# Kernel optimization log

Hardware: AMD Instinct MI355X
Metric: run time of the kernel (lower is better)

## Reference

```python
import jax, jax.numpy as jnp
import numpy as np
import math

L = 2          # gnn_num_layers
NDIM = 256     # gnn_hidden_size
H = 8          # num_heads
HH = H // 2    # heads per (full, local) split
DK = NDIM // H # 32, also == edim (relation_share_heads)
EDIM = DK
B, NPB = 32, 128
N = B * NPB            # 4096 nodes
EF = B * NPB * NPB     # 524288 complete-graph edges
EL = 131072            # local-graph edges
ELG = 262144           # line-graph edges
R = 128                # relation vocab


def _ln(x, g, b, eps=1e-5):
    m = x.mean(-1, keepdims=True)
    v = ((x - m) ** 2).mean(-1, keepdims=True)
    return (x - m) / jnp.sqrt(v + eps) * g + b


def _ffn(x, W1, b1, W2, b2, g, b):
    h = jax.nn.relu(x @ W1 + b1)
    return _ln(x + h @ W2 + b2, g, b)


def _edge_attn(q, k, v, e, src, dst, n_seg):
    """Relation-aware graph attention (DGL propagate_attention + edge_softmax).
    q,k,v: [n_seg,h,d]; e: [E,h,d] edge-relation bias or None; src,dst: [E].
    score_e = ((k[src]+e) . q[dst]) / sqrt(d); softmax over in-edges of dst;
    out[dst] = sum alpha_e * (v[src]+e)."""
    ks = k[src] + e if e is not None else k[src]          # [E,h,d]
    vs = v[src] + e if e is not None else v[src]          # [E,h,d]
    s = jnp.einsum('ehd,ehd->eh', ks, q[dst]) / math.sqrt(q.shape[-1])
    smax = jax.ops.segment_max(s, dst, num_segments=n_seg)
    ex = jnp.exp(s - jnp.maximum(smax, -1e30)[dst])
    den = jax.ops.segment_sum(ex, dst, num_segments=n_seg)[dst]
    alpha = ex / jnp.where(den > 0, den, 1.0)
    return jax.ops.segment_sum(alpha[..., None] * vs, dst, num_segments=n_seg)


def _model(x, rel_embed,
           n_Wq, n_bq, n_Wk, n_bk, n_Wv, n_bv, n_Wo, n_bo, n_ln_g, n_ln_b,
           n_f_W1, n_f_b1, n_f_W2, n_f_b2, n_f_ln_g, n_f_ln_b,
           e_Wsrc, e_Wdst, e_Wq, e_bq, e_Wk, e_Wv, e_Wo, e_bo, e_ln_g, e_ln_b,
           e_f_W1, e_f_b1, e_f_W2, e_f_b2, e_f_ln_g, e_f_ln_b,
           full_src, full_dst, g_src, g_dst, lg_src, lg_dst, edge_feat, full_edge_feat):
    lg_x = rel_embed[edge_feat]            # [EL, EDIM]  (shared embedding)
    lg_x_full = rel_embed[full_edge_feat]  # [EF, EDIM]  (fixed across layers)
    n, el, ef = x.shape[0], lg_x.shape[0], lg_x_full.shape[0]
    for i in range(L):
        # ---------- node update: first HH heads on full graph, last HH on local ----------
        q = (x @ n_Wq[i] + n_bq[i]).reshape(n, H, DK)
        k = (x @ n_Wk[i] + n_bk[i]).reshape(n, H, DK)
        v = (x @ n_Wv[i] + n_bv[i]).reshape(n, H, DK)
        # edim == d_k -> relation bias broadcast across heads (the expand branch)
        e_full = jnp.broadcast_to(lg_x_full[:, None, :], (ef, HH, DK))
        e_loc = jnp.broadcast_to(lg_x[:, None, :], (el, HH, DK))
        o1 = _edge_attn(q[:, :HH], k[:, :HH], v[:, :HH], e_full, full_src, full_dst, n)
        o2 = _edge_attn(q[:, HH:], k[:, HH:], v[:, HH:], e_loc, g_src, g_dst, n)
        o = jnp.concatenate([o1, o2], axis=1).reshape(n, NDIM)
        x_new = _ln(x + o @ n_Wo[i] + n_bo[i], n_ln_g[i], n_ln_b[i])
        x_new = _ffn(x_new, n_f_W1[i], n_f_b1[i], n_f_W2[i], n_f_b2[i], n_f_ln_g[i], n_f_ln_b[i])
        # ---------- edge update on line graph, conditioned on PRE-update src/dst node feats ----------
        mixed = lg_x + x[g_src] @ e_Wsrc[i] + x[g_dst] @ e_Wdst[i]  # [EL, EDIM]
        dke = EDIM // H
        eq = (mixed @ e_Wq[i] + e_bq[i]).reshape(el, H, dke)
        ek = (mixed @ e_Wk[i]).reshape(el, H, dke)
        ev = (mixed @ e_Wv[i]).reshape(el, H, dke)
        ow = _edge_attn(eq, ek, ev, None, lg_src, lg_dst, el).reshape(el, EDIM)
        lg_new = _ln(lg_x + ow @ e_Wo[i] + e_bo[i], e_ln_g[i], e_ln_b[i])
        lg_new = _ffn(lg_new, e_f_W1[i], e_f_b1[i], e_f_W2[i], e_f_b2[i], e_f_ln_g[i], e_f_ln_b[i])
        x, lg_x = x_new, lg_new
    return x, lg_x


def setup_inputs() -> dict:
    key = jax.random.key(0)
    ki = iter(jax.random.split(key, 48))
    def p(shape, scale=0.05):
        return jax.random.normal(next(ki), shape, dtype=jnp.float32) * scale
    rng = np.random.default_rng(0)
    blk = (np.arange(B, dtype=np.int32) * NPB)
    ii, jj = np.meshgrid(np.arange(NPB, dtype=np.int32), np.arange(NPB, dtype=np.int32), indexing='ij')
    full_src = (blk[:, None, None] + ii[None]).reshape(-1)   # block-diagonal complete graph
    full_dst = (blk[:, None, None] + jj[None]).reshape(-1)
    epb = EL // B
    g_src = (np.repeat(blk, epb) + rng.integers(0, NPB, EL)).astype(np.int32)
    g_dst = (np.repeat(blk, epb) + rng.integers(0, NPB, EL)).astype(np.int32)
    lpb = ELG // B
    eblk = np.arange(B, dtype=np.int32) * epb
    lg_src = (np.repeat(eblk, lpb) + rng.integers(0, epb, ELG)).astype(np.int32)
    lg_dst = (np.repeat(eblk, lpb) + rng.integers(0, epb, ELG)).astype(np.int32)
    return dict(
        x=jax.random.normal(next(ki), (N, NDIM), dtype=jnp.float32),
        rel_embed=p((R, EDIM), 1.0),
        full_src=jnp.asarray(full_src), full_dst=jnp.asarray(full_dst),
        g_src=jnp.asarray(g_src), g_dst=jnp.asarray(g_dst),
        lg_src=jnp.asarray(lg_src), lg_dst=jnp.asarray(lg_dst),
        edge_feat=jnp.asarray(rng.integers(0, R, EL).astype(np.int32)),
        full_edge_feat=jnp.asarray(rng.integers(0, R, EF).astype(np.int32)),
        n_Wq=p((L, NDIM, NDIM)), n_bq=p((L, NDIM)),
        n_Wk=p((L, NDIM, NDIM)), n_bk=p((L, NDIM)),
        n_Wv=p((L, NDIM, NDIM)), n_bv=p((L, NDIM)),
        n_Wo=p((L, NDIM, NDIM)), n_bo=p((L, NDIM)),
        n_ln_g=jnp.ones((L, NDIM), jnp.float32), n_ln_b=jnp.zeros((L, NDIM), jnp.float32),
        n_f_W1=p((L, NDIM, 4 * NDIM)), n_f_b1=p((L, 4 * NDIM)),
        n_f_W2=p((L, 4 * NDIM, NDIM)), n_f_b2=p((L, NDIM)),
        n_f_ln_g=jnp.ones((L, NDIM), jnp.float32), n_f_ln_b=jnp.zeros((L, NDIM), jnp.float32),
        e_Wsrc=p((L, NDIM, EDIM)), e_Wdst=p((L, NDIM, EDIM)),
        e_Wq=p((L, EDIM, EDIM)), e_bq=p((L, EDIM)),
        e_Wk=p((L, EDIM, EDIM)), e_Wv=p((L, EDIM, EDIM)),
        e_Wo=p((L, EDIM, EDIM)), e_bo=p((L, EDIM)),
        e_ln_g=jnp.ones((L, EDIM), jnp.float32), e_ln_b=jnp.zeros((L, EDIM), jnp.float32),
        e_f_W1=p((L, EDIM, 4 * EDIM)), e_f_b1=p((L, 4 * EDIM)),
        e_f_W2=p((L, 4 * EDIM, EDIM)), e_f_b2=p((L, EDIM)),
        e_f_ln_g=jnp.ones((L, EDIM), jnp.float32), e_f_ln_b=jnp.zeros((L, EDIM), jnp.float32),
    )


def reference(x, rel_embed, full_src, full_dst, g_src, g_dst, lg_src, lg_dst,
              edge_feat, full_edge_feat,
              n_Wq, n_bq, n_Wk, n_bk, n_Wv, n_bv, n_Wo, n_bo, n_ln_g, n_ln_b,
              n_f_W1, n_f_b1, n_f_W2, n_f_b2, n_f_ln_g, n_f_ln_b,
              e_Wsrc, e_Wdst, e_Wq, e_bq, e_Wk, e_Wv, e_Wo, e_bo, e_ln_g, e_ln_b,
              e_f_W1, e_f_b1, e_f_W2, e_f_b2, e_f_ln_g, e_f_ln_b):
    return _model(x, rel_embed,
                  n_Wq, n_bq, n_Wk, n_bk, n_Wv, n_bv, n_Wo, n_bo, n_ln_g, n_ln_b,
                  n_f_W1, n_f_b1, n_f_W2, n_f_b2, n_f_ln_g, n_f_ln_b,
                  e_Wsrc, e_Wdst, e_Wq, e_bq, e_Wk, e_Wv, e_Wo, e_bo, e_ln_g, e_ln_b,
                  e_f_W1, e_f_b1, e_f_W2, e_f_b2, e_f_ln_g, e_f_ln_b,
                  full_src, full_dst, g_src, g_dst, lg_src, lg_dst, edge_feat, full_edge_feat)
```

## Files before the change

kernel.cpp:

```cpp
#include <hip/hip_runtime.h>
#include <hip/hip_bf16.h>

typedef __hip_bfloat16 bf16;
typedef unsigned short ush;

static constexpr int kN   = 4096;
static constexpr int kND  = 256;
static constexpr int kEL  = 131072;
static constexpr int kED  = 32;
static constexpr int kELG = 262144;
static constexpr int kL   = 2;
static constexpr int kQW  = 832;
static constexpr int kKV  = 576;
static constexpr float kScaleN = 0.17677669529663687f;

using frag_ab = __attribute__((ext_vector_type(8))) short;
using frag_cd = __attribute__((ext_vector_type(4))) float;

__device__ __forceinline__ float ldf(const void* p, size_t i, int isbf){
    return isbf ? __bfloat162float(((const bf16*)p)[i]) : ((const float*)p)[i];
}
__device__ __forceinline__ ush f2b(float f){ bf16 h = __float2bfloat16(f); return *(ush*)&h; }
__device__ __forceinline__ float b2f(ush u){ return __uint_as_float(((unsigned)u)<<16); }
__device__ __forceinline__ ush ldb(const void* p, size_t i, int isbf){
// ... 140 lines not shown
__global__ __launch_bounds__(256) void scan_blk2_k(
    const int* __restrict__ cntL, const int* __restrict__ cntG,
    int* __restrict__ rowL, int* __restrict__ rowG, int* __restrict__ bsum)
{
    __shared__ int s[256];
    const int t = threadIdx.x;
    const bool isL = blockIdx.x < 4;
    const int* cnt = isL ? cntL : cntG;
    int* out = isL ? rowL : rowG;
    const int blk = isL ? blockIdx.x : blockIdx.x - 4;
    const int n = isL ? kN : kEL;
    const int b0 = blk*1024;
    int v[4], pre[4], tsum = 0;
    #pragma unroll
    for (int j=0;j<4;++j){
        int idx = b0 + t*4 + j;
        v[j] = (idx < n) ? cnt[idx] : 0;
        pre[j] = tsum; tsum += v[j];
    }
    s[t] = tsum; __syncthreads();
    for (int off=1; off<256; off<<=1){
        int x = (t>=off) ? s[t-off] : 0;
        __syncthreads();
        s[t] += x;
        __syncthreads();
    }
    int texc = s[t] - tsum;
    #pragma unroll
    for (int j=0;j<4;++j){
        int idx = b0 + t*4 + j;
        if (idx < n) out[idx] = texc + pre[j];
    }
    if (t == 255) bsum[(isL ? 0 : 8) + blk] = s[255];
}
__global__ __launch_bounds__(256) void scan_top2_k(int* __restrict__ bsum){
    __shared__ int sL[256], sG[256];
    const int t = threadIdx.x;
    int vL = (t < 4)   ? bsum[t]     : 0;
    int vG = (t < 128) ? bsum[8 + t] : 0;
    sL[t] = vL; sG[t] = vG; __syncthreads();
    for (int off=1; off<256; off<<=1){
        int xL = (t>=off) ? sL[t-off] : 0;
        int xG = (t>=off) ? sG[t-off] : 0;
        __syncthreads();
        sL[t] += xL; sG[t] += xG;
        __syncthreads();
    }
    if (t < 4)   bsum[t]     = sL[t] - vL;
    if (t < 128) bsum[8 + t] = sG[t] - vG;
}
__global__ void scan_add2_k(int* __restrict__ rowL, int* __restrict__ rowG,
                            const int* __restrict__ bsum,
                            int* __restrict__ curL, int* __restrict__ curG){
    int g = blockIdx.x*256 + threadIdx.x;
    if (g < kN){ int v = rowL[g] + bsum[g >> 10]; rowL[g] = v; curL[g] = v; }
    else if (g < kN + kEL){ int gg = g - kN;
        int v = rowG[gg] + bsum[8 + (gg >> 10)]; rowG[gg] = v; curG[gg] = v; }
    if (g == 0){ rowL[kN] = kEL; rowG[kEL] = kELG; }
}
__global__ void fill2_k(const int* __restrict__ gd, const int* __restrict__ lgd,
                        int* __restrict__ curL, int* __restrict__ curG,
                        int* __restrict__ eidL, int* __restrict__ eidG){
    int g = blockIdx.x*256 + threadIdx.x;
    if (g < kEL){ int pos = atomicAdd(&curL[gd[g]], 1); eidL[pos] = g; }
    else if (g < kEL + kELG){ int gg = g - kEL;
        int pos = atomicAdd(&curG[lgd[gg]], 1); eidG[pos] = gg; }
}

__global__ __launch_bounds__(256) void mgemm_k(
    const float* __restrict__ A, const ush* __restrict__ WT,
    const void* __restrict__ bias, size_t boff,
    float* __restrict__ C, const int* __restrict__ flag,
    int M, int N, int K, int flags, ush* __restrict__ aux)
{
    __shared__ __align__(16) ush As[64*72];
    __shared__ __align__(16) ush Ws[64*72];
    const int isbf = *flag;
    const int t = threadIdx.x;
    const int m0 = blockIdx.y*64, n0 = blockIdx.x*64;
    const int wave = t>>6, lane = t&63;
    const int quad = lane>>4, l15 = lane&15;
    const int r = t>>3, kq = (t&7)*8;
    const bool abf = flags & 32;

    frag_cd acc[4];
    #pragma unroll
    for (int tl=0; tl<4; ++tl)
        #pragma unroll
        for (int j=0;j<4;++j) acc[tl][j] = 0.f;

    const float* ap0 = A + (size_t)(m0+r)*K + kq;
    const float* ap1 = A + (size_t)(m0+r+32)*K + kq;
    const ush*   ab0 = (const ush*)A + (size_t)(m0+r)*K + kq;
    const ush*   ab1 = (const ush*)A + (size_t)(m0+r+32)*K + kq;
    const ush*   wp0 = WT + (size_t)(n0+r)*K + kq;
    const ush*   wp1 = WT + (size_t)(n0+r+32)*K + kq;

    float4 a00,a01,a10,a11; uint4 av0,av1, wv0,wv1;
    auto loadT = [&](int kk){
        if (abf) { av0 = *(const uint4*)(ab0+kk); av1 = *(const uint4*)(ab1+kk); }
        else { a00 = *(const float4*)(ap0+kk); a01 = *(const float4*)(ap0+kk+4);
               a10 = *(const float4*)(ap1+kk); a11 = *(const float4*)(ap1+kk+4); }
        wv0 = *(const uint4*)(wp0+kk); wv1 = *(const uint4*)(wp1+kk);
    };
    loadT(0);

    for (int kk = 0; kk < K; kk += 64) {
        if (abf) {
            *(uint4*)&As[r*72 + kq]        = av0;
            *(uint4*)&As[(r+32)*72 + kq]   = av1;
        } else {
            *(ushort4*)&As[r*72 + kq]       = make_ushort4(f2b(a00.x),f2b(a00.y),f2b(a00.z),f2b(a00.w));
            *(ushort4*)&As[r*72 + kq + 4]   = make_ushort4(f2b(a01.x),f2b(a01.y),f2b(a01.z),f2b(a01.w));
            *(ushort4*)&As[(r+32)*72 + kq]     = make_ushort4(f2b(a10.x),f2b(a10.y),f2b(a10.z),f2b(a10.w));
            *(ushort4*)&As[(r+32)*72 + kq + 4] = make_ushort4(f2b(a11.x),f2b(a11.y),f2b(a11.z),f2b(a11.w));
        }
        *(uint4*)&Ws[r*72 + kq]      = wv0;
        *(uint4*)&Ws[(r+32)*72 + kq] = wv1;
        __syncthreads();
        if (kk + 64 < K) loadT(kk + 64);
        frag_ab af0 = *(const frag_ab*)&As[(wave*16 + l15)*72 + quad*8];
        frag_ab af1 = *(const frag_ab*)&As[(wave*16 + l15)*72 + 32 + quad*8];
        #pragma unroll
        for (int tl = 0; tl < 4; ++tl) {
            frag_ab bf0 = *(const frag_ab*)&Ws[(tl*16 + l15)*72 + quad*8];
            acc[tl] = __builtin_amdgcn_mfma_f32_16x16x32_bf16(af0, bf0, acc[tl], 0, 0, 0);
            frag_ab bf1 = *(const frag_ab*)&Ws[(tl*16 + l15)*72 + 32 + quad*8];
            acc[tl] = __builtin_amdgcn_mfma_f32_16x16x32_bf16(af1, bf1, acc[tl], 0, 0, 0);
        }
        __syncthreads();
    }
    const bool do_relu = flags & 2;
    const bool has_b   = flags & 4;
    const bool obf     = flags & 8;
    #pragma unroll
    for (int tl = 0; tl < 4; ++tl) {
        int col = n0 + tl*16 + l15;
        float bv = 0.f;
        if (has_b) bv = (flags & 16) ? ((const float*)bias)[boff + col]
                                     : ldf(bias, boff + col, isbf);
        #pragma unroll
        for (int rg = 0; rg < 4; ++rg) {
            int row = m0 + wave*16 + quad*4 + rg;
            float v = acc[tl][rg] + bv;
            if (do_relu) v = fmaxf(v, 0.f);
            if (flags & 64) {
                if (col < 256) C[(size_t)row*256 + col] = v;
                else           aux[(size_t)row*kKV + (col - 256)] = f2b(v);
            } else if (obf) ((ush*)C)[(size_t)row*N + col] = f2b(v);
            else            C[(size_t)row*N + col] = v;
        }
    }
}

__global__ __launch_bounds__(256) void ln_k(
    const float* __restrict__ a, const float* __restrict__ b,
    const void* __restrict__ g, const void* __restrict__ be, size_t goff,
    float* __restrict__ out, ush* __restrict__ outb,
    const int* __restrict__ flag, int D)
{
    const int isbf = *flag;
    const int row = blockIdx.x*4 + (threadIdx.x >> 6);
    const int t = threadIdx.x & 63;
    float v[4];
    int cnt = 0;
    float s = 0.f;
    for (int i = t; i < D; i += 64) {
        float x = a[(size_t)row*D + i];
        if (b) x += b[(size_t)row*D + i];
        v[cnt++] = x; s += x;
    }
    #pragma unroll
    for (int off = 32; off > 0; off >>= 1) s += __shfl_down(s, off);
    s = __shfl(s, 0);
    const float mean = s / D;
    float qq = 0.f;
    for (int c2 = 0; c2 < cnt; ++c2) { float d = v[c2]-mean; qq += d*d; }
    #pragma unroll
    for (int off = 32; off > 0; off >>= 1) qq += __shfl_down(qq, off);
    qq = __shfl(qq, 0);
    const float inv = rsqrtf(fmaxf(qq, 0.f) / D + 1e-5f);
    cnt = 0;
    for (int i = t; i < D; i += 64) {
        float r = (v[cnt++] - mean)*inv*ldf(g, goff + i, isbf) + ldf(be, goff + i, isbf);
        out[(size_t)row*D + i] = r;
        outb[(size_t)row*D + i] = f2b(r);
    }
}

__global__ __launch_bounds__(256) void eqkv_mfma_k(
    const ush* __restrict__ lg, const ush* __restrict__ kv,
    const int* __restrict__ gsrc, const int* __restrict__ gdst,
    const ush* __restrict__ WQKV, size_t woff,
    const void* __restrict__ bq, size_t boff,
    ush* __restrict__ eq, ush* __restrict__ ek, ush* __restrict__ ev,
    const int* __restrict__ flag)
{
    __shared__ __align__(16) ush mixs[128*40];
    __shared__ __align__(16) ush wts[3][32*40];
    __shared__ float bqs[32];
    const int isbf = *flag;
    const int t = threadIdx.x;
    const int e0 = blockIdx.x * 128;
    #pragma unroll
    for (int i = t; i < 768; i += 256) {
        int m = i >> 8, r2 = i & 255;
        int n = r2 >> 3, k4 = (r2 & 7) * 4;
        *(ushort4*)&wts[m][n*40 + k4] =
            *(const ushort4*)&WQKV[(size_t)m*2048 + woff + (size_t)n*32 + k4];
    }
    if (t < 32) bqs[t] = ldf(bq, boff + t, isbf);
    {
        int r = t >> 1, c0 = (t & 1) * 16;
        int e = e0 + r;
        int s = gsrc[e], d2 = gdst[e];
        const ush* lp = lg + (size_t)e*32 + c0;
        const ush* sp = kv + (size_t)s*kKV + 512 + c0;
        const ush* dp = kv + (size_t)d2*kKV + 544 + c0;
        #pragma unroll
        for (int j = 0; j < 16; ++j)
            mixs[r*40 + c0 + j] = f2b(b2f(lp[j]) + b2f(sp[j]) + b2f(dp[j]));
    }
    __syncthreads();
    const int wave = t >> 6, l15 = t & 15, quad = (t >> 4) & 3;
    #pragma unroll
    for (int mi = 0; mi < 2; ++mi) {
        const int mt = wave*2 + mi;
        frag_ab af = *(const frag_ab*)&mixs[(mt*16 + l15)*40 + quad*8];
        #pragma unroll
        for (int w = 0; w < 3; ++w) {
            ush* outp = (w==0) ? eq : ((w==1) ? ek : ev);
            #pragma unroll
            for (int nt = 0; nt < 2; ++nt) {
                frag_ab bf = *(const frag_ab*)&wts[w][(nt*16 + l15)*40 + quad*8];
                frag_cd acc = {0.f, 0.f, 0.f, 0.f};
                acc = __builtin_amdgcn_mfma_f32_16x16x32_bf16(af, bf, acc, 0, 0, 0);
                const float bv = (w==0) ? bqs[nt*16 + l15] : 0.f;
                #pragma unroll
                for (int rg = 0; rg < 4; ++rg) {
                    int row = e0 + mt*16 + quad*4 + rg;
                    outp[(size_t)row*32 + nt*16 + l15] = f2b(acc[rg] + bv);
                }
            }
        }
    }
}

__global__ __launch_bounds__(256) void effn_mfma_k(
    const ush* __restrict__ A,
    const ush* __restrict__ W1T, size_t w1off, const void* __restrict__ b1, size_t b1off,
    const ush* __restrict__ W2T, size_t w2off, const void* __restrict__ b2, size_t b2off,
    const void* __restrict__ g, const void* __restrict__ be, size_t goff,
    ush* __restrict__ out, const int* __restrict__ flag)
{
    __shared__ __align__(16) ush w1t[128*40];
    __shared__ __align__(16) ush w2t[32*136];
    __shared__ __align__(16) ush hid[64*136];
    __shared__ float b1s[128], b2s[32];
    const int isbf = *flag;
    const int t = threadIdx.x;
    const int wave = t >> 6, l15 = t & 15, quad = (t >> 4) & 3;

    #pragma unroll
    for (int i = t; i < 1024; i += 256) {
        int n1 = i >> 3, k4 = (i & 7) * 4;
        *(ushort4*)&w1t[n1*40 + k4] = *(const ushort4*)&W1T[w1off + (size_t)n1*32 + k4];
        int n2 = i >> 5, kq2 = (i & 31) * 4;
        *(ushort4*)&w2t[n2*136 + kq2] = *(const ushort4*)&W2T[w2off + (size_t)n2*128 + kq2];
    }
    if (t < 128) b1s[t] = ldf(b1, b1off + t, isbf);
    if (t < 32)  b2s[t] = ldf(b2, b2off + t, isbf);
    __syncthreads();

    const float g0  = ldf(g,  goff + l15, isbf),      g1v = ldf(g,  goff + 16 + l15, isbf);
    const float be0 = ldf(be, goff + l15, isbf),      be1 = ldf(be, goff + 16 + l15, isbf);
    const float bb0 = b2s[l15], bb1 = b2s[16 + l15];

    for (int tt = 0; tt < 2; ++tt) {
        const int e0 = (blockIdx.x*2 + tt) * 64;
        {
            const int m = wave*16 + l15;
            frag_ab af = *(const frag_ab*)&A[(size_t)(e0+m)*32 + quad*8];
            #pragma unroll
            for (int nt = 0; nt < 8; ++nt) {
                frag_ab bf = *(const frag_ab*)&w1t[(nt*16 + l15)*40 + quad*8];
                frag_cd acc = {0.f, 0.f, 0.f, 0.f};
                acc = __builtin_amdgcn_mfma_f32_16x16x32_bf16(af, bf, acc, 0, 0, 0);
                float bv = b1s[nt*16 + l15];
                #pragma unroll
                for (int rg = 0; rg < 4; ++rg) {
                    int row = wave*16 + quad*4 + rg;
                    hid[row*136 + nt*16 + l15] = f2b(fmaxf(acc[rg] + bv, 0.f));
                }
            }
        }
        frag_cd acc2[2] = {{0.f,0.f,0.f,0.f},{0.f,0.f,0.f,0.f}};
        #pragma unroll
        for (int ks = 0; ks < 4; ++ks) {
            frag_ab af2 = *(const frag_ab*)&hid[(wave*16 + l15)*136 + ks*32 + quad*8];
            #pragma unroll
            for (int tl = 0; tl < 2; ++tl) {
                frag_ab bf2 = *(const frag_ab*)&w2t[(tl*16 + l15)*136 + ks*32 + quad*8];
                acc2[tl] = __builtin_amdgcn_mfma_f32_16x16x32_bf16(af2, bf2, acc2[tl], 0, 0, 0);
            }
        }
        #pragma unroll
        for (int rg = 0; rg < 4; ++rg) {
            const int row = e0 + wave*16 + quad*4 + rg;
            float v0 = acc2[0][rg] + bb0 + b2f(A[(size_t)row*32 + l15]);
            float v1 = acc2[1][rg] + bb1 + b2f(A[(size_t)row*32 + 16 + l15]);
            float s = v0 + v1;
            s += __shfl_xor(s,1); s += __shfl_xor(s,2); s += __shfl_xor(s,4); s += __shfl_xor(s,8);
            const float mean = s * (1.f/32.f);
            float q = (v0-mean)*(v0-mean) + (v1-mean)*(v1-mean);
            q += __shfl_xor(q,1); q += __shfl_xor(q,2); q += __shfl_xor(q,4); q += __shfl_xor(q,8);
            const float inv = rsqrtf(q * (1.f/32.f) + 1e-5f);
            out[(size_t)row*32 + l15]      = f2b((v0-mean)*inv*g0  + be0);
            out[(size_t)row*32 + 16 + l15] = f2b((v1-mean)*inv*g1v + be1);
        }
    }
}

__global__ __launch_bounds__(512) void full_attn_k(
    const float* __restrict__ q, const ush* __restrict__ kv,
    const void* __restrict__ rel, const int* __restrict__ feat, ush* __restrict__ o,
    const int* __restrict__ flag)
{
    __shared__ __align__(8) ush ks[128][36];
    __shared__ __align__(8) ush vs[128][36];
    __shared__ __align__(8) ush rs[128][36];
    __shared__ float pb[8][32][34];
    const int isbf = *flag;
    const int bid = blockIdx.x;
    const int b = bid >> 4, h = (bid >> 2) & 3, qtr = bid & 3;
    const int t = threadIdx.x;
    for (int i = t; i < 4096; i += 512) {
        int r = i >> 5, d = i & 31;
        rs[r][d] = ldb(rel, i, isbf);
        const ush* kvrow = kv + (size_t)(b*128 + r)*kKV + h*32 + d;
        ks[r][d] = kvrow[0];
        vs[r][d] = kvrow[256];
    }
    __syncthreads();
    const int wave = t >> 6, lane = t & 63;
    const int dstL = lane >> 1, part = lane & 1;
    const int dst = qtr*32 + dstL;
    const int dbase = part*16;
    float qr[16];
    { size_t base = ((size_t)(b*128 + dst))*256 + h*32 + dbase;
      #pragma unroll
      for (int d=0; d<16; ++d) qr[d] = q[base + d]; }
    const int* fp = feat + (size_t)b*16384 + dst;
    const int s0 = wave*16;
    float m = -1e30f, l = 0.f;
    float acc[16];
    #pragma unroll
    for (int d=0; d<16; ++d) acc[d] = 0.f;
    int f = fp[s0*128];
    for (int sI = 0; sI < 16; ++sI) {
        const int s = s0 + sI;
        int fn = (sI+1 < 16) ? fp[(s+1)*128] : 0;
        float er[16];
        float scp = 0.f;
        #pragma unroll
        for (int j2 = 0; j2 < 4; ++j2) {
            ushort4 eu = *(const ushort4*)&rs[f][dbase + j2*4];
            ushort4 ku = *(const ushort4*)&ks[s][dbase + j2*4];
            float e0 = b2f(eu.x), e1 = b2f(eu.y), e2 = b2f(eu.z), e3 = b2f(eu.w);
            er[j2*4+0]=e0; er[j2*4+1]=e1; er[j2*4+2]=e2; er[j2*4+3]=e3;
            scp += (b2f(ku.x)+e0)*qr[j2*4+0] + (b2f(ku.y)+e1)*qr[j2*4+1]
                 + (b2f(ku.z)+e2)*qr[j2*4+2] + (b2f(ku.w)+e3)*qr[j2*4+3];
        }
        const float sc = (scp + __shfl_xor(scp, 1)) * kScaleN;
        float mn = fmaxf(m, sc);
        float c0 = __expf(m - mn);
        float pp = __expf(sc - mn);
        l = l*c0 + pp;
        #pragma unroll
        for (int j2 = 0; j2 < 4; ++j2) {
            ushort4 vu = *(const ushort4*)&vs[s][dbase + j2*4];
            acc[j2*4+0] = acc[j2*4+0]*c0 + pp*(b2f(vu.x)+er[j2*4+0]);
            acc[j2*4+1] = acc[j2*4+1]*c0 + pp*(b2f(vu.y)+er[j2*4+1]);
            acc[j2*4+2] = acc[j2*4+2]*c0 + pp*(b2f(vu.z)+er[j2*4+2]);
            acc[j2*4+3] = acc[j2*4+3]*c0 + pp*(b2f(vu.w)+er[j2*4+3]);
        }
        m = mn; f = fn;
    }
    if (part == 0) { pb[wave][dstL][0] = m; pb[wave][dstL][1] = l; }
    #pragma unroll
    for (int d=0; d<16; ++d) pb[wave][dstL][2 + dbase + d] = acc[d];
    __syncthreads();
    {
        const int dstL2 = t & 31, grp = t >> 5;
        float mw[8], lw[8];
        #pragma unroll
        for (int w=0; w<8; ++w){ mw[w]=pb[w][dstL2][0]; lw[w]=pb[w][dstL2][1]; }
        float M = mw[0];
        #pragma unroll
        for (int w=1; w<8; ++w) M = fmaxf(M, mw[w]);
        float sw[8];
        float L = 0.f;
        #pragma unroll
        for (int w=0; w<8; ++w){ sw[w] = __expf(mw[w]-M); L += lw[w]*sw[w]; }
        const float inv = 1.f / fmaxf(L, 1e-30f);
        size_t base = ((size_t)(b*128 + qtr*32 + dstL2))*kND + h*32 + grp*2;
        #pragma unroll
        for (int d=0; d<2; ++d) {
            float a = 0.f;
            #pragma unroll
            for (int w=0; w<8; ++w) a += pb[w][dstL2][2+grp*2+d]*sw[w];
            o[base + d] = f2b(a*inv);
        }
    }
}

__global__ __launch_bounds__(256) void loc_gather_k(
    const float* __restrict__ q, const ush* __restrict__ kv,
    const ush* __restrict__ lg, const int* __restrict__ gsrc,
    const int* __restrict__ rowp, const int* __restrict__ eidl,
    ush* __restrict__ o)
{
    const int n = blockIdx.x;
    const int h = threadIdx.x >> 6;
    const int lane = threadIdx.x & 63;
    const int g = lane >> 4;
    const int d0 = (lane & 15) * 2;
    const size_t hoff = (size_t)(4 + h) * 32 + d0;
    const float2 q2 = *(const float2*)&q[(size_t)n*256 + hoff];
    const int beg = rowp[n], end = rowp[n+1];
    const int deg = end - beg;
    float m = -1e30f, l = 0.f, ax = 0.f, ay = 0.f;
    if (deg > 0) {
        const int nIter = (deg + 3) >> 2;
        int idx = beg + g;
        int ce = eidl[min(idx, end-1)];
        int cs = gsrc[ce];
        for (int it = 0; it < nIter; ++it) {
            const bool valid = idx < end;
            const int e = ce, s = cs;
            idx += 4;
            if (it + 1 < nIter) { ce = eidl[min(idx, end-1)]; cs = gsrc[ce]; }
            const ushort2 ku = *(const ushort2*)&kv[(size_t)s*kKV + 128 + h*32 + d0];
            const ushort2 lvu = *(const ushort2*)&lg[(size_t)e*32 + d0];
            const ushort2 vu = *(const ushort2*)&kv[(size_t)s*kKV + 384 + h*32 + d0];
            const float lvx = b2f(lvu.x), lvy = b2f(lvu.y);
            float part = (b2f(ku.x)+lvx)*q2.x + (b2f(ku.y)+lvy)*q2.y;
            part += __shfl_xor(part, 1);
            part += __shfl_xor(part, 2);
            part += __shfl_xor(part, 4);
            part += __shfl_xor(part, 8);
            const float sc = part * kScaleN;
            const float mn = valid ? fmaxf(m, sc) : m;
            const float c  = __expf(m - mn);
            const float pp = valid ? __expf(sc - mn) : 0.f;
            l  = l*c  + pp;
            ax = ax*c + pp*(b2f(vu.x)+lvx);
            ay = ay*c + pp*(b2f(vu.y)+lvy);
            m  = mn;
        }
        #pragma unroll
        for (int off = 16; off <= 32; off <<= 1) {
            const float mo = __shfl_xor(m, off);
            const float lo = __shfl_xor(l, off);
            const float xo = __shfl_xor(ax, off);
            const float yo = __shfl_xor(ay, off);
            const float M  = fmaxf(m, mo);
            const float c1 = __expf(m - M);
            const float c2 = __expf(mo - M);
            l  = l*c1  + lo*c2;
            ax = ax*c1 + xo*c2;
            ay = ay*c1 + yo*c2;
            m  = M;
        }
    }
    if (g == 0) {
        const float inv = 1.f / fmaxf(l, 1e-30f);
        *(ushort2*)&o[(size_t)n*kND + hoff] = make_ushort2(f2b(ax*inv), f2b(ay*inv));
    }
}

__global__ __launch_bounds__(256) void lgs_ewo_k(
    const ush* __restrict__ eq, const ush* __restrict__ ek, const ush* __restrict__ ev,
    const int* __restrict__ lsrc, const int* __restrict__ rowp, const int* __restrict__ eidl,
    const ush* __restrict__ res,
    const ush* __restrict__ WO, size_t wooff, const void* __restrict__ bo, size_t booff,
    const void* __restrict__ g1, const void* __restrict__ be1, size_t g1off,
    ush* __restrict__ out, const int* __restrict__ flag)
{
    __shared__ __align__(16) ush ows[32*40];
    __shared__ __align__(16) ush wos[32*40];
    __shared__ float cs[32][36];
    __shared__ float bos[32], gs[32], bs[32];
    const int isbf = *flag;
    const int t = threadIdx.x;
    const int base = blockIdx.x * 32;
    {
        int n = t >> 3, k4 = (t & 7) * 4;
        *(ushort4*)&wos[n*40 + k4] = *(const ushort4*)&WO[wooff + (size_t)n*32 + k4];
    }
    if (t < 32) {
        bos[t] = ldf(bo, booff + t, isbf);
        gs[t]  = ldf(g1, g1off + t, isbf);
        bs[t]  = ldf(be1, g1off + t, isbf);
    }
    {
        const int d2 = base + (t >> 3), h = t & 7;
        const ushort4 qu = *(const ushort4*)&eq[(size_t)d2*32 + h*4];
        const float q0 = b2f(qu.x), q1 = b2f(qu.y), q2 = b2f(qu.z), q3 = b2f(qu.w);
        const int beg = rowp[d2], end = rowp[d2+1];
        float m = -1e30f, l = 0.f;
        float4 acc = make_float4(0.f,0.f,0.f,0.f);
        int i = beg;
        int s = 0;
        if (i < end) { s = lsrc[eidl[i]]; }
        while (i < end) {
            const int sc_s = s;
            ++i;
            if (i < end) { s = lsrc[eidl[i]]; }
            const ushort4 ku = *(const ushort4*)&ek[(size_t)sc_s*32 + h*4];
            const ushort4 vu = *(const ushort4*)&ev[(size_t)sc_s*32 + h*4];
            float sc = (b2f(ku.x)*q0 + b2f(ku.y)*q1 + b2f(ku.z)*q2 + b2f(ku.w)*q3) * 0.5f;
            float mn = fmaxf(m, sc);
            float c = __expf(m - mn);
            float pp = __expf(sc - mn);
            l = l*c + pp;
            acc.x = acc.x*c + pp*b2f(vu.x);
            acc.y = acc.y*c + pp*b2f(vu.y);
            acc.z = acc.z*c + pp*b2f(vu.z);
            acc.w = acc.w*c + pp*b2f(vu.w);
            m = mn;
        }
        const float inv = 1.f / fmaxf(l, 1e-30f);
        const int r = t >> 3, c0 = h*4;
        ows[r*40 + c0 + 0] = f2b(acc.x*inv);
        ows[r*40 + c0 + 1] = f2b(acc.y*inv);
        ows[r*40 + c0 + 2] = f2b(acc.z*inv);
        ows[r*40 + c0 + 3] = f2b(acc.w*inv);
    }
    __syncthreads();
    {
        const int wave = t >> 6, l15 = t & 15, quad = (t >> 4) & 3;
        const int mt = wave & 1, nt = wave >> 1;
        frag_ab af = *(const frag_ab*)&ows[(mt*16 + l15)*40 + quad*8];
        frag_ab bf = *(const frag_ab*)&wos[(nt*16 + l15)*40 + quad*8];
        frag_cd acc = {0.f, 0.f, 0.f, 0.f};
        acc = __builtin_amdgcn_mfma_f32_16x16x32_bf16(af, bf, acc, 0, 0, 0);
        #pragma unroll
        for (int rg = 0; rg < 4; ++rg) {
            const int row = mt*16 + quad*4 + rg;
            const int col = nt*16 + l15;
            cs[row][col] = acc[rg] + bos[col] + b2f(res[(size_t)(base+row)*32 + col]);
        }
    }
    __syncthreads();
    {
        const int row = t >> 3, c0 = (t & 7) * 4;
        const float v0 = cs[row][c0], v1 = cs[row][c0+1];
        const float v2 = cs[row][c0+2], v3 = cs[row][c0+3];
        float s = v0+v1+v2+v3;
        s += __shfl_xor(s,1); s += __shfl_xor(s,2); s += __shfl_xor(s,4);
        const float mean = s * (1.f/32.f);
        float qq = (v0-mean)*(v0-mean)+(v1-mean)*(v1-mean)
                 + (v2-mean)*(v2-mean)+(v3-mean)*(v3-mean);
        qq += __shfl_xor(qq,1); qq += __shfl_xor(qq,2); qq += __shfl_xor(qq,4);
        const float inv = rsqrtf(qq * (1.f/32.f) + 1e-5f);
        out[(size_t)(base+row)*32 + c0 + 0] = f2b((v0-mean)*inv*gs[c0+0] + bs[c0+0]);
        out[(size_t)(base+row)*32 + c0 + 1] = f2b((v1-mean)*inv*gs[c0+1] + bs[c0+1]);
        out[(size_t)(base+row)*32 + c0 + 2] = f2b((v2-mean)*inv*gs[c0+2] + bs[c0+2]);
        out[(size_t)(base+row)*32 + c0 + 3] = f2b((v3-mean)*inv*gs[c0+3] + bs[c0+3]);
    }
}

__global__ void out_k(const float* __restrict__ xf, const ush* __restrict__ lgf,
                      void* __restrict__ out, const int* __restrict__ flag){
    const int isbf = *flag;
    int g = blockIdx.x*256 + threadIdx.x;
    if (g < kN*kND) {
        float v = xf[g];
        if (isbf) ((ush*)out)[g] = f2b(v);
        else      ((float*)out)[g] = v;
    } else {
        ush u = lgf[g - kN*kND];
        if (isbf) ((ush*)out)[g] = u;
        else      ((float*)out)[g] = b2f(u);
    }
}

static inline void mgemm(const float* A, const ush* WT, const void* bias, size_t boff,
                         float* C, const int* flag, int M, int N, int K, int flags,
                         hipStream_t s, ush* aux){
    dim3 grid((N+63)/64, M/64);
    mgemm_k<<<grid, 256, 0, s>>>(A, WT, bias, boff, C, flag, M, N, K, flags, aux);
}

extern "C" void kernel_launch(void* const* d_in, const int* in_sizes, int n_in,
                              void* d_out, int out_size, void* d_ws, size_t ws_size,
                              hipStream_t stream) {
    const void* x_in      = d_in[0];
    const void* rel       = d_in[1];
    const int* g_src      = (const int*)d_in[4];
    const int* g_dst      = (const int*)d_in[5];
    const int* lg_src     = (const int*)d_in[6];
    const int* lg_dst     = (const int*)d_in[7];
    const int* edge_feat  = (const int*)d_in[8];
    const int* full_feat  = (const int*)d_in[9];
    const void* n_Wq   = d_in[10];
    const void* n_bq   = d_in[11];
    const void* n_Wk   = d_in[12];
    const void* n_bk   = d_in[13];
    const void* n_Wv   = d_in[14];
    const void* n_bv   = d_in[15];
    const void* n_Wo   = d_in[16];
    const void* n_bo   = d_in[17];
    const void* n_lng  = d_in[18];
    const void* n_lnb  = d_in[19];
    const void* n_fW1  = d_in[20];
    const void* n_fb1  = d_in[21];
    const void* n_fW2  = d_in[22];
    const void* n_fb2  = d_in[23];
    const void* n_flng = d_in[24];
    const void* n_flnb = d_in[25];
    const void* e_Wsrc = d_in[26];
    const void* e_Wdst = d_in[27];
    const void* e_Wq   = d_in[28];
    const void* e_bq   = d_in[29];
    const void* e_Wk   = d_in[30];
    const void* e_Wv   = d_in[31];
    const void* e_Wo   = d_in[32];
    const void* e_bo   = d_in[33];
    const void* e_lng  = d_in[34];
    const void* e_lnb  = d_in[35];
    const void* e_fW1  = d_in[36];
    const void* e_fb1  = d_in[37];
    const void* e_fW2  = d_in[38];
    const void* e_fb2  = d_in[39];
    const void* e_flng = d_in[40];
    const void* e_flnb = d_in[41];

    float* p = (float*)d_ws;
    size_t off = 0;
    auto AL = [&](size_t n){ float* r = p + off; off += n; return r; };
    int* flagp = (int*)AL(64);
    float* xA   = AL((size_t)kN*kND);
    float* xB   = AL((size_t)kN*kND);
    float* xM   = AL((size_t)kN*kND);
    ush*   xAb  = (ush*)AL((size_t)kN*kND/2);
    ush*   xBb  = (ush*)AL((size_t)kN*kND/2);
    ush*   xMb  = (ush*)AL((size_t)kN*kND/2);
    float* qkvb = AL((size_t)kN*kND);
    ush*   kvaux= (ush*)AL((size_t)kN*kKV/2);
    ush*   ob   = (ush*)AL((size_t)kN*kND/2);
    float* tN   = AL((size_t)kN*kND);
    ush*   nh   = (ush*)AL((size_t)kN*512);
    ush*   lgA  = (ush*)AL((size_t)kEL*kED/2);
    ush*   lgB  = (ush*)AL((size_t)kEL*kED/2);
    ush*   lgM  = (ush*)AL((size_t)kEL*kED/2);
    ush*   eqb  = (ush*)AL((size_t)kEL*16);
    ush*   ekb  = (ush*)AL((size_t)kEL*16);
    ush*   evb  = (ush*)AL((size_t)kEL*16);
    int* cntL  = (int*)AL(kN);
    int* rowL  = (int*)AL(kN + 64);
    int* curL  = (int*)AL(kN);
    int* eidL  = (int*)AL(kEL);
    int* cntG  = (int*)AL(kEL);
    int* rowG  = (int*)AL(kEL + 64);
    int* curG  = (int*)AL(kEL);
    int* eidG  = (int*)AL(kELG);
    int* bsum  = (int*)AL(256);
    ush* wtQKVSD = (ush*)AL(212992);
    float* bQKV  = AL(2*kQW);
    ush* wtO  = (ush*)AL(65536);
    ush* wtF1 = (ush*)AL(262144);
    ush* wtF2 = (ush*)AL(262144);
    ush* wtEQKV = (ush*)AL(3072);
    ush* wtEO   = (ush*)AL(1024);
    ush* wtEF1  = (ush*)AL(4096);
    ush* wtEF2  = (ush*)AL(4096);
    if (ws_size < off * sizeof(float)) return;

    detect_k<<<1, 64, 0, stream>>>((const ush*)x_in, flagp);
    {
        long total = (long)kN*kND + (long)kEL*kED + 2*kQW + kN + kEL;
        int blocks = (int)((total + 255) / 256);
        setup_misc_k<<<blocks, 256, 0, stream>>>(x_in, rel, edge_feat, n_bq, n_bk, n_bv,
                                                 xA, xAb, lgA, bQKV, cntL, cntG, flagp);
    }
    trans_all_k<<<6368, 256, 0, stream>>>(n_Wq, n_Wk, n_Wv, n_Wo, n_fW1, n_fW2,
                                          e_Wsrc, e_Wdst, e_Wq, e_Wk, e_Wv, e_Wo,
                                          e_fW1, e_fW2, flagp,
                                          wtQKVSD, wtO, wtF1, wtF2,
                                          wtEQKV, wtEO, wtEF1, wtEF2);

    count2_k<<<(kEL+kELG)/256, 256, 0, stream>>>(g_dst, lg_dst, cntL, cntG);
    scan_blk2_k<<<132, 256, 0, stream>>>(cntL, cntG, rowL, rowG, bsum);
    scan_top2_k<<<1, 256, 0, stream>>>(bsum);
    scan_add2_k<<<(kN+kEL)/256, 256, 0, stream>>>(rowL, rowG, bsum, curL, curG);
    fill2_k<<<(kEL+kELG)/256, 256, 0, stream>>>(g_dst, lg_dst, curL, curG, eidL, eidG);

    float* xc = xA;  float* xn = xB;
    ush* xcb = xAb;  ush* xnb = xBb;
    ush* lgc = lgA;  ush* lgn = lgB;

    for (int i = 0; i < kL; ++i) {
        const size_t o256 = (size_t)i*kND;
        const size_t o1024= (size_t)i*1024;
        const size_t o32  = (size_t)i*kED;
        const size_t o128 = (size_t)i*128;

        mgemm((const float*)xcb, wtQKVSD + (size_t)i*212992, bQKV, (size_t)i*kQW, qkvb,
              flagp, kN, kQW, kND, 4|16|32|64, stream, kvaux);
        full_attn_k<<<512, 512, 0, stream>>>(qkvb, kvaux, rel, full_feat, ob, flagp);
        loc_gather_k<<<kN, 256, 0, stream>>>(qkvb, kvaux, lgc, g_src, rowL, eidL, ob);
        mgemm((const float*)ob, wtO + (size_t)i*65536, n_bo, o256, tN, flagp,
              kN, kND, kND, 4|32, stream, nullptr);
        ln_k<<<kN/4, 256, 0, stream>>>(xc, tN, n_lng, n_lnb, o256, xM, xMb, flagp, kND);
        mgemm((const float*)xMb, wtF1 + (size_t)i*262144, n_fb1, o1024, (float*)nh, flagp,
              kN, 1024, kND, 4|2|8|32, stream, nullptr);
        mgemm((const float*)nh, wtF2 + (size_t)i*262144, n_fb2, o256, tN, flagp,
              kN, kND, 1024, 4|32, stream, nullptr);
        ln_k<<<kN/4, 256, 0, stream>>>(xM, tN, n_flng, n_flnb, o256, xn, xnb, flagp, kND);

        eqkv_mfma_k<<<kEL/128, 256, 0, stream>>>(lgc, kvaux, g_src, g_dst,
                                                 wtEQKV, (size_t)i*1024, e_bq, o32,
                                                 eqb, ekb, evb, flagp);
        lgs_ewo_k<<<kEL/32, 256, 0, stream>>>(eqb, ekb, evb, lg_src, rowG, eidG,
                                              lgc, wtEO, (size_t)i*1024, e_bo, o32,
                                              e_lng, e_lnb, o32, lgM, flagp);
        effn_mfma_k<<<kEL/128, 256, 0, stream>>>(lgM, wtEF1, (size_t)i*4096, e_fb1, o128,
                                                 wtEF2, (size_t)i*4096, e_fb2, o32,
                                                 e_flng, e_flnb, o32, lgn, flagp);

        { float* t = xc; xc = xn; xn = t; }
        { ush* t = xcb; xcb = xnb; xnb = t; }
        { ush* t = lgc; lgc = lgn; lgn = t; }
    }

    out_k<<<(kN*kND + kEL*kED)/256, 256, 0, stream>>>(xc, lgc, d_out, flagp);
}
```

Measured before the change: 523.8 us.

## Split-K node GEMMs with partial sums reduced in layernorm; merge attention kernels

The output-projection and FFN2 node GEMMs (N=256, grid of 4x64=256 blocks) now use a split-K of 2 via blockIdx.z. Each half writes its partial sum to its own buffer, and the following layernorm adds both partials, so twice as many blocks run on the GPU without atomics. The full-graph and local-graph attention kernels are also merged into one launch, saving one launch and letting the two block types overlap. In exchange the workspace grows by one extra fp32 buffer, the layernorm reads more data, and the merged kernel gives the local blocks full-attention shared-memory and 512-thread occupancy limits.

```diff
diff --git a/kernel.cpp b/kernel.cpp
--- a/kernel.cpp
+++ b/kernel.cpp
@@ -246,6 +246,9 @@
     const int quad = lane>>4, l15 = lane&15;
     const int r = t>>3, kq = (t&7)*8;
     const bool abf = flags & 32;
+    const bool spk = flags & 128;
+    const int Kc   = spk ? (K / gridDim.z) : K;
+    const int koff = spk ? (blockIdx.z * Kc) : 0;
 
     frag_cd acc[4];
     #pragma unroll
@@ -253,12 +256,12 @@
         #pragma unroll
         for (int j=0;j<4;++j) acc[tl][j] = 0.f;
 
-    const float* ap0 = A + (size_t)(m0+r)*K + kq;
-    const float* ap1 = A + (size_t)(m0+r+32)*K + kq;
-    const ush*   ab0 = (const ush*)A + (size_t)(m0+r)*K + kq;
-    const ush*   ab1 = (const ush*)A + (size_t)(m0+r+32)*K + kq;
-    const ush*   wp0 = WT + (size_t)(n0+r)*K + kq;
-    const ush*   wp1 = WT + (size_t)(n0+r+32)*K + kq;
+    const float* ap0 = A + (size_t)(m0+r)*K + koff + kq;
+    const float* ap1 = A + (size_t)(m0+r+32)*K + koff + kq;
+    const ush*   ab0 = (const ush*)A + (size_t)(m0+r)*K + koff + kq;
+    const ush*   ab1 = (const ush*)A + (size_t)(m0+r+32)*K + koff + kq;
+    const ush*   wp0 = WT + (size_t)(n0+r)*K + koff + kq;
+    const ush*   wp1 = WT + (size_t)(n0+r+32)*K + koff + kq;
 
     float4 a00,a01,a10,a11; uint4 av0,av1, wv0,wv1;
     auto loadT = [&](int kk){
@@ -269,7 +272,7 @@
     };
     loadT(0);
 
-    for (int kk = 0; kk < K; kk += 64) {
+    for (int kk = 0; kk < Kc; kk += 64) {
         if (abf) {
             *(uint4*)&As[r*72 + kq]        = av0;
             *(uint4*)&As[(r+32)*72 + kq]   = av1;
@@ -282,7 +285,7 @@
         *(uint4*)&Ws[r*72 + kq]      = wv0;
         *(uint4*)&Ws[(r+32)*72 + kq] = wv1;
         __syncthreads();
-        if (kk + 64 < K) loadT(kk + 64);
+        if (kk + 64 < Kc) loadT(kk + 64);
         frag_ab af0 = *(const frag_ab*)&As[(wave*16 + l15)*72 + quad*8];
         frag_ab af1 = *(const frag_ab*)&As[(wave*16 + l15)*72 + 32 + quad*8];
         #pragma unroll
@@ -295,8 +298,9 @@
         __syncthreads();
     }
     const bool do_relu = flags & 2;
-    const bool has_b   = flags & 4;
+    const bool has_b   = (flags & 4) && (!spk || blockIdx.z == 0);
     const bool obf     = flags & 8;
+    float* Cz = spk ? (C + (size_t)blockIdx.z * M * N) : C;
     #pragma unroll
     for (int tl = 0; tl < 4; ++tl) {
         int col = n0 + tl*16 + l15;
@@ -312,13 +316,13 @@
                 if (col < 256) C[(size_t)row*256 + col] = v;
                 else           aux[(size_t)row*kKV + (col - 256)] = f2b(v);
             } else if (obf) ((ush*)C)[(size_t)row*N + col] = f2b(v);
-            else            C[(size_t)row*N + col] = v;
+            else            Cz[(size_t)row*N + col] = v;
         }
     }
 }
 
 __global__ __launch_bounds__(256) void ln_k(
-    const float* __restrict__ a, const float* __restrict__ b,
+    const float* __restrict__ a, const float* __restrict__ b, const float* __restrict__ b2,
     const void* __restrict__ g, const void* __restrict__ be, size_t goff,
     float* __restrict__ out, ush* __restrict__ outb,
     const int* __restrict__ flag, int D)
@@ -331,7 +335,8 @@
     float s = 0.f;
     for (int i = t; i < D; i += 64) {
         float x = a[(size_t)row*D + i];
-        if (b) x += b[(size_t)row*D + i];
+        if (b)  x += b[(size_t)row*D + i];
+        if (b2) x += b2[(size_t)row*D + i];
         v[cnt++] = x; s += x;
     }
     #pragma unroll
@@ -485,10 +490,12 @@
     }
 }
 
-__global__ __launch_bounds__(512) void full_attn_k(
+__global__ __launch_bounds__(512) void attn_all_k(
     const float* __restrict__ q, const ush* __restrict__ kv,
-    const void* __restrict__ rel, const int* __restrict__ feat, ush* __restrict__ o,
-    const int* __restrict__ flag)
+    const void* __restrict__ rel, const int* __restrict__ feat,
+    const ush* __restrict__ lg, const int* __restrict__ gsrc,
+    const int* __restrict__ rowp, const int* __restrict__ eidl,
+    ush* __restrict__ o, const int* __restrict__ flag)
 {
     __shared__ __align__(8) ush ks[128][36];
     __shared__ __align__(8) ush vs[128][36];
@@ -496,150 +503,145 @@
     __shared__ float pb[8][32][34];
     const int isbf = *flag;
     const int bid = blockIdx.x;
-    const int b = bid >> 4, h = (bid >> 2) & 3, qtr = bid & 3;
     const int t = threadIdx.x;
-    for (int i = t; i < 4096; i += 512) {
-        int r = i >> 5, d = i & 31;
-        rs[r][d] = ldb(rel, i, isbf);
-        const ush* kvrow = kv + (size_t)(b*128 + r)*kKV + h*32 + d;
-        ks[r][d] = kvrow[0];
-        vs[r][d] = kvrow[256];
-    }
-    __syncthreads();
-    const int wave = t >> 6, lane = t & 63;
-    const int dstL = lane >> 1, part = lane & 1;
-    const int dst = qtr*32 + dstL;
-    const int dbase = part*16;
-    float qr[16];
-    { size_t base = ((size_t)(b*128 + dst))*256 + h*32 + dbase;
-      #pragma unroll
-      for (int d=0; d<16; ++d) qr[d] = q[base + d]; }
-    const int* fp = feat + (size_t)b*16384 + dst;
-    const int s0 = wave*16;
-    float m = -1e30f, l = 0.f;
-    float acc[16];
-    #pragma unroll
-    for (int d=0; d<16; ++d) acc[d] = 0.f;
-    int f = fp[s0*128];
-    for (int sI = 0; sI < 16; ++sI) {
-        const int s = s0 + sI;
-        int fn = (sI+1 < 16) ? fp[(s+1)*128] : 0;
-        float er[16];
-        float scp = 0.f;
+    if (bid < 512) {
+        const int b = bid >> 4, h = (bid >> 2) & 3, qtr = bid & 3;
+        for (int i = t; i < 4096; i += 512) {
+            int r = i >> 5, d = i & 31;
+            rs[r][d] = ldb(rel, i, isbf);
+            const ush* kvrow = kv + (size_t)(b*128 + r)*kKV + h*32 + d;
+            ks[r][d] = kvrow[0];
+            vs[r][d] = kvrow[256];
+        }
+        __syncthreads();
+        const int wave = t >> 6, lane = t & 63;
+        const int dstL = lane >> 1, part = lane & 1;
+        const int dst = qtr*32 + dstL;
+        const int dbase = part*16;
+        float qr[16];
+        { size_t base = ((size_t)(b*128 + dst))*256 + h*32 + dbase;
+          #pragma unroll
+          for (int d=0; d<16; ++d) qr[d] = q[base + d]; }
+        const int* fp = feat + (size_t)b*16384 + dst;
+        const int s0 = wave*16;
+        float m = -1e30f, l = 0.f;
+        float acc[16];
         #pragma unroll
-        for (int j2 = 0; j2 < 4; ++j2) {
-            ushort4 eu = *(const ushort4*)&rs[f][dbase + j2*4];
-            ushort4 ku = *(const ushort4*)&ks[s][dbase + j2*4];
-            float e0 = b2f(eu.x), e1 = b2f(eu.y), e2 = b2f(eu.z), e3 = b2f(eu.w);
-            er[j2*4+0]=e0; er[j2*4+1]=e1; er[j2*4+2]=e2; er[j2*4+3]=e3;
-            scp += (b2f(ku.x)+e0)*qr[j2*4+0] + (b2f(ku.y)+e1)*qr[j2*4+1]
-                 + (b2f(ku.z)+e2)*qr[j2*4+2] + (b2f(ku.w)+e3)*qr[j2*4+3];
-        }
-        const float sc = (scp + __shfl_xor(scp, 1)) * kScaleN;
-        float mn = fmaxf(m, sc);
-        float c0 = __expf(m - mn);
-        float pp = __expf(sc - mn);
-        l = l*c0 + pp;
+        for (int d=0; d<16; ++d) acc[d] = 0.f;
+        int f = fp[s0*128];
+        for (int sI = 0; sI < 16; ++sI) {
+            const int s = s0 + sI;
+            int fn = (sI+1 < 16) ? fp[(s+1)*128] : 0;
+            float er[16];
+            float scp = 0.f;
+            #pragma unroll
+            for (int j2 = 0; j2 < 4; ++j2) {
+                ushort4 eu = *(const ushort4*)&rs[f][dbase + j2*4];
+                ushort4 ku = *(const ushort4*)&ks[s][dbase + j2*4];
+                float e0 = b2f(eu.x), e1 = b2f(eu.y), e2 = b2f(eu.z), e3 = b2f(eu.w);
+                er[j2*4+0]=e0; er[j2*4+1]=e1; er[j2*4+2]=e2; er[j2*4+3]=e3;
+                scp += (b2f(ku.x)+e0)*qr[j2*4+0] + (b2f(ku.y)+e1)*qr[j2*4+1]
+                     + (b2f(ku.z)+e2)*qr[j2*4+2] + (b2f(ku.w)+e3)*qr[j2*4+3];
+            }
+            const float sc = (scp + __shfl_xor(scp, 1)) * kScaleN;
+            float mn = fmaxf(m, sc);
+            float c0 = __expf(m - mn);
+            float pp = __expf(sc - mn);
+            l = l*c0 + pp;
+            #pragma unroll
+            for (int j2 = 0; j2 < 4; ++j2) {
+                ushort4 vu = *(const ushort4*)&vs[s][dbase + j2*4];
+                acc[j2*4+0] = acc[j2*4+0]*c0 + pp*(b2f(vu.x)+er[j2*4+0]);
+                acc[j2*4+1] = acc[j2*4+1]*c0 + pp*(b2f(vu.y)+er[j2*4+1]);
+                acc[j2*4+2] = acc[j2*4+2]*c0 + pp*(b2f(vu.z)+er[j2*4+2]);
+                acc[j2*4+3] = acc[j2*4+3]*c0 + pp*(b2f(vu.w)+er[j2*4+3]);
+            }
+            m = mn; f = fn;
+        }
+        if (part == 0) { pb[wave][dstL][0] = m; pb[wave][dstL][1] = l; }
         #pragma unroll
-        for (int j2 = 0; j2 < 4; ++j2) {
-            ushort4 vu = *(const ushort4*)&vs[s][dbase + j2*4];
-            acc[j2*4+0] = acc[j2*4+0]*c0 + pp*(b2f(vu.x)+er[j2*4+0]);
-            acc[j2*4+1] = acc[j2*4+1]*c0 + pp*(b2f(vu.y)+er[j2*4+1]);
-            acc[j2*4+2] = acc[j2*4+2]*c0 + pp*(b2f(vu.z)+er[j2*4+2]);
-            acc[j2*4+3] = acc[j2*4+3]*c0 + pp*(b2f(vu.w)+er[j2*4+3]);
-        }
-        m = mn; f = fn;
-    }
-    if (part == 0) { pb[wave][dstL][0] = m; pb[wave][dstL][1] = l; }
-    #pragma unroll
-    for (int d=0; d<16; ++d) pb[wave][dstL][2 + dbase + d] = acc[d];
-    __syncthreads();
-    {
-        const int dstL2 = t & 31, grp = t >> 5;
-        float mw[8], lw[8];
-        #pragma unroll
-        for (int w=0; w<8; ++w){ mw[w]=pb[w][dstL2][0]; lw[w]=pb[w][dstL2][1]; }
-        float M = mw[0];
-        #pragma unroll
-        for (int w=1; w<8; ++w) M = fmaxf(M, mw[w]);
-        float sw[8];
-        float L = 0.f;
-        #pragma unroll
-        for (int w=0; w<8; ++w){ sw[w] = __expf(mw[w]-M); L += lw[w]*sw[w]; }
-        const float inv = 1.f / fmaxf(L, 1e-30f);
-        size_t base = ((size_t)(b*128 + qtr*32 + dstL2))*kND + h*32 + grp*2;
-        #pragma unroll
-        for (int d=0; d<2; ++d) {
-            float a = 0.f;
+        for (int d=0; d<16; ++d) pb[wave][dstL][2 + dbase + d] = acc[d];
+        __syncthreads();
+        {
+            const int dstL2 = t & 31, grp = t >> 5;
+            float mw[8], lw[8];
             #pragma unroll
-            for (int w=0; w<8; ++w) a += pb[w][dstL2][2+grp*2+d]*sw[w];
-            o[base + d] = f2b(a*inv);
-        }
-    }
-}
-
-__global__ __launch_bounds__(256) void loc_gather_k(
-    const float* __restrict__ q, const ush* __restrict__ kv,
-    const ush* __restrict__ lg, const int* __restrict__ gsrc,
-    const int* __restrict__ rowp, const int* __restrict__ eidl,
-    ush* __restrict__ o)
-{
-    const int n = blockIdx.x;
-    const int h = threadIdx.x >> 6;
-    const int lane = threadIdx.x & 63;
-    const int g = lane >> 4;
-    const int d0 = (lane & 15) * 2;
-    const size_t hoff = (size_t)(4 + h) * 32 + d0;
-    const float2 q2 = *(const float2*)&q[(size_t)n*256 + hoff];
-    const int beg = rowp[n], end = rowp[n+1];
-    const int deg = end - beg;
-    float m = -1e30f, l = 0.f, ax = 0.f, ay = 0.f;
-    if (deg > 0) {
-        const int nIter = (deg + 3) >> 2;
-        int idx = beg + g;
-        int ce = eidl[min(idx, end-1)];
-        int cs = gsrc[ce];
-        for (int it = 0; it < nIter; ++it) {
-            const bool valid = idx < end;
-            const int e = ce, s = cs;
-            idx += 4;
-            if (it + 1 < nIter) { ce = eidl[min(idx, end-1)]; cs = gsrc[ce]; }
-            const ushort2 ku = *(const ushort2*)&kv[(size_t)s*kKV + 128 + h*32 + d0];
-            const ushort2 lvu = *(const ushort2*)&lg[(size_t)e*32 + d0];
-            const ushort2 vu = *(const ushort2*)&kv[(size_t)s*kKV + 384 + h*32 + d0];
-            const float lvx = b2f(lvu.x), lvy = b2f(lvu.y);
-            float part = (b2f(ku.x)+lvx)*q2.x + (b2f(ku.y)+lvy)*q2.y;
-            part += __shfl_xor(part, 1);
-            part += __shfl_xor(part, 2);
-            part += __shfl_xor(part, 4);
-            part += __shfl_xor(part, 8);
-            const float sc = part * kScaleN;
-            const float mn = valid ? fmaxf(m, sc) : m;
-            const float c  = __expf(m - mn);
-            const float pp = valid ? __expf(sc - mn) : 0.f;
-            l  = l*c  + pp;
-            ax = ax*c + pp*(b2f(vu.x)+lvx);
-            ay = ay*c + pp*(b2f(vu.y)+lvy);
-            m  = mn;
-        }
-        #pragma unroll
-        for (int off = 16; off <= 32; off <<= 1) {
-            const float mo = __shfl_xor(m, off);
-            const float lo = __shfl_xor(l, off);
-            const float xo = __shfl_xor(ax, off);
-            const float yo = __shfl_xor(ay, off);
-            const float M  = fmaxf(m, mo);
-            const float c1 = __expf(m - M);
-            const float c2 = __expf(mo - M);
-            l  = l*c1  + lo*c2;
-            ax = ax*c1 + xo*c2;
-            ay = ay*c1 + yo*c2;
-            m  = M;
-        }
-    }
-    if (g == 0) {
-        const float inv = 1.f / fmaxf(l, 1e-30f);
-        *(ushort2*)&o[(size_t)n*kND + hoff] = make_ushort2(f2b(ax*inv), f2b(ay*inv));
+            for (int w=0; w<8; ++w){ mw[w]=pb[w][dstL2][0]; lw[w]=pb[w][dstL2][1]; }
+            float M = mw[0];
+            #pragma unroll
+            for (int w=1; w<8; ++w) M = fmaxf(M, mw[w]);
+            float sw[8];
+            float L = 0.f;
+            #pragma unroll
+            for (int w=0; w<8; ++w){ sw[w] = __expf(mw[w]-M); L += lw[w]*sw[w]; }
+            const float inv = 1.f / fmaxf(L, 1e-30f);
+            size_t base = ((size_t)(b*128 + qtr*32 + dstL2))*kND + h*32 + grp*2;
+            #pragma unroll
+            for (int d=0; d<2; ++d) {
+                float a = 0.f;
+                #pragma unroll
+                for (int w=0; w<8; ++w) a += pb[w][dstL2][2+grp*2+d]*sw[w];
+                o[base + d] = f2b(a*inv);
+            }
+        }
+    } else {
+        const int n = (bid - 512)*2 + (t >> 8);
+        const int h = (t >> 6) & 3;
+        const int lane = t & 63;
+        const int g = lane >> 4;
+        const int d0 = (lane & 15) * 2;
+        const size_t hoff = (size_t)(4 + h) * 32 + d0;
+        const float2 q2 = *(const float2*)&q[(size_t)n*256 + hoff];
+        const int beg = rowp[n], end = rowp[n+1];
+        const int deg = end - beg;
+        float m = -1e30f, l = 0.f, ax = 0.f, ay = 0.f;
+        if (deg > 0) {
+            const int nIter = (deg + 3) >> 2;
+            int idx = beg + g;
+            int ce = eidl[min(idx, end-1)];
+            int cs = gsrc[ce];
+            for (int it = 0; it < nIter; ++it) {
+                const bool valid = idx < end;
+                const int e = ce, s = cs;
+                idx += 4;
+                if (it + 1 < nIter) { ce = eidl[min(idx, end-1)]; cs = gsrc[ce]; }
+                const ushort2 ku = *(const ushort2*)&kv[(size_t)s*kKV + 128 + h*32 + d0];
+                const ushort2 lvu = *(const ushort2*)&lg[(size_t)e*32 + d0];
+                const ushort2 vu = *(const ushort2*)&kv[(size_t)s*kKV + 384 + h*32 + d0];
+                const float lvx = b2f(lvu.x), lvy = b2f(lvu.y);
+                float part = (b2f(ku.x)+lvx)*q2.x + (b2f(ku.y)+lvy)*q2.y;
+                part += __shfl_xor(part, 1);
+                part += __shfl_xor(part, 2);
+                part += __shfl_xor(part, 4);
+                part += __shfl_xor(part, 8);
+                const float sc = part * kScaleN;
+                const float mn = valid ? fmaxf(m, sc) : m;
+                const float c  = __expf(m - mn);
+                const float pp = valid ? __expf(sc - mn) : 0.f;
+                l  = l*c  + pp;
+                ax = ax*c + pp*(b2f(vu.x)+lvx);
+                ay = ay*c + pp*(b2f(vu.y)+lvy);
+                m  = mn;
+            }
+            #pragma unroll
+            for (int off = 16; off <= 32; off <<= 1) {
+                const float mo = __shfl_xor(m, off);
+                const float lo = __shfl_xor(l, off);
+                const float xo = __shfl_xor(ax, off);
+                const float yo = __shfl_xor(ay, off);
+                const float M  = fmaxf(m, mo);
+                const float c1 = __expf(m - M);
+                const float c2 = __expf(mo - M);
+                l  = l*c1  + lo*c2;
+                ax = ax*c1 + xo*c2;
+                ay = ay*c1 + yo*c2;
+                m  = M;
+            }
+        }
+        if (g == 0) {
+            const float inv = 1.f / fmaxf(l, 1e-30f);
+            *(ushort2*)&o[(size_t)n*kND + hoff] = make_ushort2(f2b(ax*inv), f2b(ay*inv));
+        }
     }
 }
 
@@ -752,8 +754,8 @@
 
 static inline void mgemm(const float* A, const ush* WT, const void* bias, size_t boff,
                          float* C, const int* flag, int M, int N, int K, int flags,
-                         hipStream_t s, ush* aux){
-    dim3 grid((N+63)/64, M/64);
+                         hipStream_t s, ush* aux, int splitz = 1){
+    dim3 grid((N+63)/64, M/64, splitz);
     mgemm_k<<<grid, 256, 0, s>>>(A, WT, bias, boff, C, flag, M, N, K, flags, aux);
 }
 
@@ -814,7 +816,7 @@
     float* qkvb = AL((size_t)kN*kND);
     ush*   kvaux= (ush*)AL((size_t)kN*kKV/2);
     ush*   ob   = (ush*)AL((size_t)kN*kND/2);
-    float* tN   = AL((size_t)kN*kND);
+    float* tN   = AL((size_t)kN*kND*2);
     ush*   nh   = (ush*)AL((size_t)kN*512);
     ush*   lgA  = (ush*)AL((size_t)kEL*kED/2);
     ush*   lgB  = (ush*)AL((size_t)kEL*kED/2);
@@ -842,6 +844,8 @@
     ush* wtEF2  = (ush*)AL(4096);
     if (ws_size < off * sizeof(float)) return;
 
+    float* tN2 = tN + (size_t)kN*kND;
+
     detect_k<<<1, 64, 0, stream>>>((const ush*)x_in, flagp);
     {
         long total = (long)kN*kND + (long)kEL*kED + 2*kQW + kN + kEL;
@@ -873,16 +877,16 @@
 
         mgemm((const float*)xcb, wtQKVSD + (size_t)i*212992, bQKV, (size_t)i*kQW, qkvb,
               flagp, kN, kQW, kND, 4|16|32|64, stream, kvaux);
-        full_attn_k<<<512, 512, 0, stream>>>(qkvb, kvaux, rel, full_feat, ob, flagp);
-        loc_gather_k<<<kN, 256, 0, stream>>>(qkvb, kvaux, lgc, g_src, rowL, eidL, ob);
+        attn_all_k<<<512 + kN/2, 512, 0, stream>>>(qkvb, kvaux, rel, full_feat,
+                                                   lgc, g_src, rowL, eidL, ob, flagp);
         mgemm((const float*)ob, wtO + (size_t)i*65536, n_bo, o256, tN, flagp,
-              kN, kND, kND, 4|32, stream, nullptr);
-        ln_k<<<kN/4, 256, 0, stream>>>(xc, tN, n_lng, n_lnb, o256, xM, xMb, flagp, kND);
+              kN, kND, kND, 4|32|128, stream, nullptr, 2);
+        ln_k<<<kN/4, 256, 0, stream>>>(xc, tN, tN2, n_lng, n_lnb, o256, xM, xMb, flagp, kND);
         mgemm((const float*)xMb, wtF1 + (size_t)i*262144, n_fb1, o1024, (float*)nh, flagp,
               kN, 1024, kND, 4|2|8|32, stream, nullptr);
         mgemm((const float*)nh, wtF2 + (size_t)i*262144, n_fb2, o256, tN, flagp,
-              kN, kND, 1024, 4|32, stream, nullptr);
-        ln_k<<<kN/4, 256, 0, stream>>>(xM, tN, n_flng, n_flnb, o256, xn, xnb, flagp, kND);
+              kN, kND, 1024, 4|32|128, stream, nullptr, 2);
+        ln_k<<<kN/4, 256, 0, stream>>>(xM, tN, tN2, n_flng, n_flnb, o256, xn, xnb, flagp, kND);
 
         eqkv_mfma_k<<<kEL/128, 256, 0, stream>>>(lgc, kvaux, g_src, g_dst,
                                                  wtEQKV, (size_t)i*1024, e_bq, o32,
```

Result: slower. 548.3 us (+4.7%).
